# Kernel optimization log

Hardware: AMD Instinct MI355X
Metric: run time of the kernel (lower is better)

## Reference

```python
import jax, jax.numpy as jnp
import numpy as np

T, H, I, E = 4096, 1024, 512, 16


def setup_inputs() -> dict:
    key = jax.random.key(0)
    k1, k2, k3 = jax.random.split(key, 3)
    x = jax.random.normal(k1, (T, H), dtype=jnp.float32)
    gate_up_proj = jax.random.normal(k2, (E, H, 2 * I), dtype=jnp.float32) * 0.02
    down_proj = jax.random.normal(k3, (E, I, H), dtype=jnp.float32) * 0.02
    # uneven expert token counts summing exactly to T (no padding rows)
    rng = np.random.default_rng(0)
    raw = rng.integers(64, 512, size=E)
    counts = (raw * T) // raw.sum()
    counts[-1] += T - counts.sum()
    num_tokens_per_expert = jnp.asarray(counts, dtype=jnp.int32)
    return {"x": x, "gate_up_proj": gate_up_proj, "down_proj": down_proj,
            "num_tokens_per_expert": num_tokens_per_expert}


def reference(x, gate_up_proj, down_proj, num_tokens_per_expert):
    # tokens are sorted by expert; build per-token expert id (jit-safe: fixed length)
    n_tok = x.shape[0]
    n_exp = gate_up_proj.shape[0]
    seg = jnp.repeat(jnp.arange(n_exp), num_tokens_per_expert, total_repeat_length=n_tok)  # [T]

    def body(acc, ew):
        e, w_gu, w_d = ew
        xe = jnp.where((seg == e)[:, None], x, jnp.zeros((), x.dtype))  # [T, H], zero rows for other experts
        gu = xe @ w_gu                                                  # [T, 2I]
        g, u = jnp.split(gu, 2, axis=-1)
        o = (jax.nn.silu(g) * u) @ w_d                                  # [T, H]; masked rows stay exactly 0
        return acc + o, None

    init = jnp.zeros((n_tok, down_proj.shape[-1]), x.dtype)
    out, _ = jax.lax.scan(body, init, (jnp.arange(n_exp), gate_up_proj, down_proj))
    return out
```

## Files before the change

kernel.cpp:

```cpp
#include <hip/hip_runtime.h>
#include <hip/hip_bf16.h>

#define T_TOK 4096
#define H_DIM 1024
#define I_DIM 512
#define E_EXP 16
#define BM    128
#define BK    64
#define BSTR  68

using bf16x8   = __attribute__((ext_vector_type(8))) short;
using floatx4  = __attribute__((ext_vector_type(4))) float;
using ushort4v = __attribute__((ext_vector_type(4))) unsigned short;

__device__ __forceinline__ unsigned short f2bf(float f) {
  union { float f; unsigned u; } v; v.f = f;
  return (unsigned short)((v.u + 0x7FFFu + ((v.u >> 16) & 1u)) >> 16);
}
__device__ __forceinline__ unsigned pk2(float a, float b) {
  return (unsigned)f2bf(a) | ((unsigned)f2bf(b) << 16);
}

__device__ __forceinline__ void gld16(const void* g, void* l) {
  __builtin_amdgcn_global_load_lds((const __attribute__((address_space(1))) void*)g,
                                   (__attribute__((address_space(3))) void*)l,
                                   16, 0, 0);
}

__device__ __forceinline__ bool tile_info(const int* __restrict__ counts, int by,
                                          int& e, int& row0, int& base, int& cnt) {
  int acc = 0, off = 0;
  e = -1;
  #pragma unroll
  for (int i = 0; i < E_EXP; ++i) {
    int c = counts[i];
    int nt = (c + BM - 1) >> 7;
    if (e < 0 && by < acc + nt) { e = i; row0 = (by - acc) * BM; base = off; cnt = c; }
    acc += nt; off += c;
  }
  return e >= 0;
}

__global__ void k_cvt(const float* __restrict__ x, unsigned short* __restrict__ xb) {
  const float4* s4 = (const float4*)x;
  int b0 = blockIdx.x * 512 + threadIdx.x;
  float4 a = s4[b0];
  float4 b = s4[b0 + 256];
  ushort4v oa, ob;
  oa.x = f2bf(a.x); oa.y = f2bf(a.y); oa.z = f2bf(a.z); oa.w = f2bf(a.w);
  ob.x = f2bf(b.x); ob.y = f2bf(b.y); ob.z = f2bf(b.z); ob.w = f2bf(b.w);
  ((ushort4v*)xb)[b0] = oa;
  ((ushort4v*)xb)[b0 + 256] = ob;
}

__launch_bounds__(256, 3)
__global__ void k_gemm_a(const unsigned short* __restrict__ xb,
                         const float* __restrict__ wgu,
                         unsigned short* __restrict__ hb,
                         const int* __restrict__ counts) {
  __shared__ unsigned short As[BM * BK];
  __shared__ unsigned short Bs[BM * BSTR];

  int e, row0, base, cnt;
  if (!tile_info(counts, blockIdx.y, e, row0, base, cnt)) return;
  const int rows = (cnt - row0 < BM) ? (cnt - row0) : BM;
  const int c0 = blockIdx.x * 64;

  const int tid = threadIdx.x;
  const int w = tid >> 6, l = tid & 63;
  const int lr = l & 15, q = l >> 4;
  const int asr = l >> 3, akc = (l & 7) * 8;
  const int nloc = ((w & 1) << 6) | l;
  const int kh = (w >> 1) * 32;
  const int gcol = (nloc < 64) ? (c0 + nloc) : (I_DIM + c0 + (nloc - 64));
  const float* wcol = wgu + (size_t)e * H_DIM * (2 * I_DIM) + gcol;
  unsigned int* BsD = (unsigned int*)Bs;
  const int bdst = nloc * (BSTR / 2) + (kh >> 1);

  const int mhalf = w & 1, nhalf = w >> 1;
  const int mrow = mhalf * 64;

  floatx4 accg[4][2], accu[4][2];
  #pragma unroll
  for (int i = 0; i < 4; ++i)
    #pragma unroll
    for (int j = 0; j < 2; ++j) { accg[i][j] = (floatx4){0,0,0,0}; accu[i][j] = (floatx4){0,0,0,0}; }

  const int nk = H_DIM / BK;
  for (int ki = 0; ki < nk; ++ki) {
    const int kk = ki * BK;
    float bv[32];
    #pragma unroll
    for (int j = 0; j < 32; ++j)
      bv[j] = wcol[(size_t)(kk + kh + j) * (2 * I_DIM)];
    #pragma unroll
    for (int t = 0; t < 4; ++t) {
      int r = w * 32 + t * 8 + asr;
      int gr = r < rows ? r : rows - 1;
      gld16(&xb[(size_t)(base + row0 + gr) * H_DIM + kk + akc], &As[(w * 32 + t * 8) * BK]);
    }
    #pragma unroll
    for (int jq = 0; jq < 8; ++jq) {
      uint2 d;
      d.x = pk2(bv[4 * jq + 0], bv[4 * jq + 1]);
      d.y = pk2(bv[4 * jq + 2], bv[4 * jq + 3]);
      *(uint2*)&BsD[bdst + jq * 2] = d;
    }
    __syncthreads();
    #pragma unroll
    for (int kf = 0; kf < 2; ++kf) {
      const int ch = (kf * 4 + q) * 8;
      bf16x8 af[4], bg[2], bu[2];
      #pragma unroll
      for (int mi = 0; mi < 4; ++mi)
        af[mi] = *(const bf16x8*)&As[(mrow + mi * 16 + lr) * BK + ch];
      #pragma unroll
      for (int ni = 0; ni < 2; ++ni) {
        bg[ni] = *(const bf16x8*)&Bs[(nhalf * 32 + ni * 16 + lr) * BSTR + ch];
        bu[ni] = *(const bf16x8*)&Bs[(64 + nhalf * 32 + ni * 16 + lr) * BSTR + ch];
      }
      #pragma unroll
      for (int mi = 0; mi < 4; ++mi)
        #pragma unroll
        for (int ni = 0; ni < 2; ++ni) {
          accg[mi][ni] = __builtin_amdgcn_mfma_f32_16x16x32_bf16(af[mi], bg[ni], accg[mi][ni], 0, 0, 0);
          accu[mi][ni] = __builtin_amdgcn_mfma_f32_16x16x32_bf16(af[mi], bu[ni], accu[mi][ni], 0, 0, 0);
        }
    }
    __syncthreads();
  }

  #pragma unroll
  for (int mi = 0; mi < 4; ++mi)
    #pragma unroll
    for (int r = 0; r < 4; ++r) {
      int row_local = mrow + mi * 16 + q * 4 + r;
      if (row_local >= rows) continue;
      size_t orow = (size_t)(base + row0 + row_local) * I_DIM;
      #pragma unroll
      for (int ni = 0; ni < 2; ++ni) {
        float g = accg[mi][ni][r], u = accu[mi][ni][r];
        float s = g / (1.0f + __expf(-g)) * u;
        hb[orow + c0 + nhalf * 32 + ni * 16 + lr] = f2bf(s);
      }
    }
}

__launch_bounds__(256, 3)
__global__ void k_gemm_b(const unsigned short* __restrict__ hb,
                         const float* __restrict__ wdn,
                         float* __restrict__ out,
                         const int* __restrict__ counts) {
  __shared__ unsigned short As[BM * BK];
  __shared__ unsigned short Bs[BM * BSTR];

  int e, row0, base, cnt;
  if (!tile_info(counts, blockIdx.y, e, row0, base, cnt)) return;
  const int rows = (cnt - row0 < BM) ? (cnt - row0) : BM;
  const int n0 = blockIdx.x * 128;

  const int tid = threadIdx.x;
  const int w = tid >> 6, l = tid & 63;
  const int lr = l & 15, q = l >> 4;
  const int asr = l >> 3, akc = (l & 7) * 8;
  const int nloc = ((w & 1) << 6) | l;
  const int kh = (w >> 1) * 32;
  const float* wcol = wdn + (size_t)e * I_DIM * H_DIM + n0 + nloc;
  unsigned int* BsD = (unsigned int*)Bs;
  const int bdst = nloc * (BSTR / 2) + (kh >> 1);

  const int mhalf = w & 1, nhalf = w >> 1;
  const int mrow = mhalf * 64;

  floatx4 acc[4][4];
  #pragma unroll
  for (int i = 0; i < 4; ++i)
    #pragma unroll
    for (int j = 0; j < 4; ++j) acc[i][j] = (floatx4){0,0,0,0};

  const int nk = I_DIM / BK;
  for (int ki = 0; ki < nk; ++ki) {
    const int kk = ki * BK;
    float bv[32];
    #pragma unroll
    for (int j = 0; j < 32; ++j)
      bv[j] = wcol[(size_t)(kk + kh + j) * H_DIM];
    #pragma unroll
    for (int t = 0; t < 4; ++t) {
      int r = w * 32 + t * 8 + asr;
      int gr = r < rows ? r : rows - 1;
      gld16(&hb[(size_t)(base + row0 + gr) * I_DIM + kk + akc], &As[(w * 32 + t * 8) * BK]);
    }
    #pragma unroll
    for (int jq = 0; jq < 8; ++jq) {
      uint2 d;
      d.x = pk2(bv[4 * jq + 0], bv[4 * jq + 1]);
      d.y = pk2(bv[4 * jq + 2], bv[4 * jq + 3]);
      *(uint2*)&BsD[bdst + jq * 2] = d;
    }
    __syncthreads();
    #pragma unroll
    for (int kf = 0; kf < 2; ++kf) {
      const int ch = (kf * 4 + q) * 8;
      bf16x8 af[4], bf[4];
      #pragma unroll
      for (int mi = 0; mi < 4; ++mi)
        af[mi] = *(const bf16x8*)&As[(mrow + mi * 16 + lr) * BK + ch];
      #pragma unroll
      for (int ni = 0; ni < 4; ++ni)
        bf[ni] = *(const bf16x8*)&Bs[(nhalf * 64 + ni * 16 + lr) * BSTR + ch];
      #pragma unroll
      for (int mi = 0; mi < 4; ++mi)
        #pragma unroll
        for (int ni = 0; ni < 4; ++ni)
          acc[mi][ni] = __builtin_amdgcn_mfma_f32_16x16x32_bf16(af[mi], bf[ni], acc[mi][ni], 0, 0, 0);
    }
    __syncthreads();
  }

  #pragma unroll
  for (int mi = 0; mi < 4; ++mi)
    #pragma unroll
    for (int r = 0; r < 4; ++r) {
      int row_local = mrow + mi * 16 + q * 4 + r;
      if (row_local >= rows) continue;
      size_t orow = (size_t)(base + row0 + row_local) * H_DIM;
      #pragma unroll
      for (int ni = 0; ni < 4; ++ni)
        out[orow + n0 + nhalf * 64 + ni * 16 + lr] = acc[mi][ni][r];
    }
}

extern "C" void kernel_launch(void* const* d_in, const int* in_sizes, int n_in,
                              void* d_out, int out_size, void* d_ws, size_t ws_size,
                              hipStream_t stream) {
  const float* x      = (const float*)d_in[0];
  const float* wgu    = (const float*)d_in[1];
  const float* wdn    = (const float*)d_in[2];
  const int*   counts = (const int*)d_in[3];
  float* out = (float*)d_out;

  unsigned char* ws = (unsigned char*)d_ws;
  unsigned short* xb = (unsigned short*)(ws);
  unsigned short* hb = (unsigned short*)(ws + 8388608);

  k_cvt<<<2048, 256, 0, stream>>>(x, xb);
  k_gemm_a<<<dim3(I_DIM / 64, 48), 256, 0, stream>>>(xb, wgu, hb, counts);
  k_gemm_b<<<dim3(H_DIM / 128, 48), 256, 0, stream>>>(hb, wdn, out, counts);
}
```

Measured before the change: 182.0 us.

## Double-buffer A tiles and prefetch weights to overlap loads with MFMA

Both grouped GEMM kernels now prefetch the next K-slice (fp32 weights into registers, bf16 activations into a second LDS buffer via global_load_lds) before computing on the current slice. The goal is to hide global memory latency behind MFMA work. The A tile in LDS also gets an XOR swizzle on 16-byte chunks to cut bank conflicts on fragment reads. The cost is more LDS per block, which may lower occupancy below the launch-bounds target, plus two barriers per iteration.

```diff
diff --git a/kernel.cpp b/kernel.cpp
--- a/kernel.cpp
+++ b/kernel.cpp
@@ -1,5 +1,4 @@
 #include <hip/hip_runtime.h>
-#include <hip/hip_bf16.h>
 
 #define T_TOK 4096
 #define H_DIM 1024
@@ -58,7 +57,7 @@
                          const float* __restrict__ wgu,
                          unsigned short* __restrict__ hb,
                          const int* __restrict__ counts) {
-  __shared__ unsigned short As[BM * BK];
+  __shared__ unsigned short As[2][BM * BK];
   __shared__ unsigned short Bs[BM * BSTR];
 
   int e, row0, base, cnt;
@@ -69,7 +68,9 @@
   const int tid = threadIdx.x;
   const int w = tid >> 6, l = tid & 63;
   const int lr = l & 15, q = l >> 4;
-  const int asr = l >> 3, akc = (l & 7) * 8;
+  const int asr = l >> 3;
+  const int akc = ((l & 7) ^ asr) * 8;
+  const int cswz = lr & 7;
   const int nloc = ((w & 1) << 6) | l;
   const int kh = (w >> 1) * 32;
   const int gcol = (nloc < 64) ? (c0 + nloc) : (I_DIM + c0 + (nloc - 64));
@@ -79,6 +80,14 @@
 
   const int mhalf = w & 1, nhalf = w >> 1;
   const int mrow = mhalf * 64;
+  const unsigned short* arow = xb + (size_t)(base + row0) * H_DIM;
+
+  int agr[4];
+  #pragma unroll
+  for (int t = 0; t < 4; ++t) {
+    int r = w * 32 + t * 8 + asr;
+    agr[t] = (r < rows) ? r : rows - 1;
+  }
 
   floatx4 accg[4][2], accu[4][2];
   #pragma unroll
@@ -86,34 +95,32 @@
     #pragma unroll
     for (int j = 0; j < 2; ++j) { accg[i][j] = (floatx4){0,0,0,0}; accu[i][j] = (floatx4){0,0,0,0}; }
 
-  const int nk = H_DIM / BK;
-  for (int ki = 0; ki < nk; ++ki) {
-    const int kk = ki * BK;
-    float bv[32];
-    #pragma unroll
-    for (int j = 0; j < 32; ++j)
-      bv[j] = wcol[(size_t)(kk + kh + j) * (2 * I_DIM)];
-    #pragma unroll
-    for (int t = 0; t < 4; ++t) {
-      int r = w * 32 + t * 8 + asr;
-      int gr = r < rows ? r : rows - 1;
-      gld16(&xb[(size_t)(base + row0 + gr) * H_DIM + kk + akc], &As[(w * 32 + t * 8) * BK]);
-    }
-    #pragma unroll
-    for (int jq = 0; jq < 8; ++jq) {
-      uint2 d;
-      d.x = pk2(bv[4 * jq + 0], bv[4 * jq + 1]);
-      d.y = pk2(bv[4 * jq + 2], bv[4 * jq + 3]);
-      *(uint2*)&BsD[bdst + jq * 2] = d;
-    }
-    __syncthreads();
+  float bv[32];
+
+  #pragma unroll
+  for (int j = 0; j < 32; ++j) bv[j] = wcol[(size_t)(kh + j) * (2 * I_DIM)];
+  #pragma unroll
+  for (int t = 0; t < 4; ++t)
+    gld16(&arow[(size_t)agr[t] * H_DIM + akc], &As[0][(w * 32 + t * 8) * BK]);
+  #pragma unroll
+  for (int jq = 0; jq < 8; ++jq) {
+    uint2 d;
+    d.x = pk2(bv[4 * jq + 0], bv[4 * jq + 1]);
+    d.y = pk2(bv[4 * jq + 2], bv[4 * jq + 3]);
+    *(uint2*)&BsD[bdst + jq * 2] = d;
+  }
+  __syncthreads();
+
+  auto compute = [&](int cb) {
     #pragma unroll
     for (int kf = 0; kf < 2; ++kf) {
-      const int ch = (kf * 4 + q) * 8;
+      const int c = kf * 4 + q;
+      const int ca = (c ^ cswz) * 8;
+      const int ch = c * 8;
       bf16x8 af[4], bg[2], bu[2];
       #pragma unroll
       for (int mi = 0; mi < 4; ++mi)
-        af[mi] = *(const bf16x8*)&As[(mrow + mi * 16 + lr) * BK + ch];
+        af[mi] = *(const bf16x8*)&As[cb][(mrow + mi * 16 + lr) * BK + ca];
       #pragma unroll
       for (int ni = 0; ni < 2; ++ni) {
         bg[ni] = *(const bf16x8*)&Bs[(nhalf * 32 + ni * 16 + lr) * BSTR + ch];
@@ -127,8 +134,30 @@
           accu[mi][ni] = __builtin_amdgcn_mfma_f32_16x16x32_bf16(af[mi], bu[ni], accu[mi][ni], 0, 0, 0);
         }
     }
+  };
+
+  const int nk = H_DIM / BK;
+  int cur = 0;
+  for (int ki = 0; ki < nk - 1; ++ki) {
+    const int kk = (ki + 1) * BK;
+    #pragma unroll
+    for (int j = 0; j < 32; ++j) bv[j] = wcol[(size_t)(kk + kh + j) * (2 * I_DIM)];
+    #pragma unroll
+    for (int t = 0; t < 4; ++t)
+      gld16(&arow[(size_t)agr[t] * H_DIM + kk + akc], &As[cur ^ 1][(w * 32 + t * 8) * BK]);
+    compute(cur);
     __syncthreads();
-  }
+    #pragma unroll
+    for (int jq = 0; jq < 8; ++jq) {
+      uint2 d;
+      d.x = pk2(bv[4 * jq + 0], bv[4 * jq + 1]);
+      d.y = pk2(bv[4 * jq + 2], bv[4 * jq + 3]);
+      *(uint2*)&BsD[bdst + jq * 2] = d;
+    }
+    __syncthreads();
+    cur ^= 1;
+  }
+  compute(cur);
 
   #pragma unroll
   for (int mi = 0; mi < 4; ++mi)
@@ -151,7 +180,7 @@
                          const float* __restrict__ wdn,
                          float* __restrict__ out,
                          const int* __restrict__ counts) {
-  __shared__ unsigned short As[BM * BK];
+  __shared__ unsigned short As[2][BM * BK];
   __shared__ unsigned short Bs[BM * BSTR];
 
   int e, row0, base, cnt;
@@ -162,7 +191,9 @@
   const int tid = threadIdx.x;
   const int w = tid >> 6, l = tid & 63;
   const int lr = l & 15, q = l >> 4;
-  const int asr = l >> 3, akc = (l & 7) * 8;
+  const int asr = l >> 3;
+  const int akc = ((l & 7) ^ asr) * 8;
+  const int cswz = lr & 7;
   const int nloc = ((w & 1) << 6) | l;
   const int kh = (w >> 1) * 32;
   const float* wcol = wdn + (size_t)e * I_DIM * H_DIM + n0 + nloc;
@@ -171,6 +202,14 @@
 
   const int mhalf = w & 1, nhalf = w >> 1;
   const int mrow = mhalf * 64;
+  const unsigned short* arow = hb + (size_t)(base + row0) * I_DIM;
+
+  int agr[4];
+  #pragma unroll
+  for (int t = 0; t < 4; ++t) {
+    int r = w * 32 + t * 8 + asr;
+    agr[t] = (r < rows) ? r : rows - 1;
+  }
 
   floatx4 acc[4][4];
   #pragma unroll
@@ -178,19 +217,54 @@
     #pragma unroll
     for (int j = 0; j < 4; ++j) acc[i][j] = (floatx4){0,0,0,0};
 
+  float bv[32];
+
+  #pragma unroll
+  for (int j = 0; j < 32; ++j) bv[j] = wcol[(size_t)(kh + j) * H_DIM];
+  #pragma unroll
+  for (int t = 0; t < 4; ++t)
+    gld16(&arow[(size_t)agr[t] * I_DIM + akc], &As[0][(w * 32 + t * 8) * BK]);
+  #pragma unroll
+  for (int jq = 0; jq < 8; ++jq) {
+    uint2 d;
+    d.x = pk2(bv[4 * jq + 0], bv[4 * jq + 1]);
+    d.y = pk2(bv[4 * jq + 2], bv[4 * jq + 3]);
+    *(uint2*)&BsD[bdst + jq * 2] = d;
+  }
+  __syncthreads();
+
+  auto compute = [&](int cb) {
+    #pragma unroll
+    for (int kf = 0; kf < 2; ++kf) {
+      const int c = kf * 4 + q;
+      const int ca = (c ^ cswz) * 8;
+      const int ch = c * 8;
+      bf16x8 af[4], bf[4];
+      #pragma unroll
+      for (int mi = 0; mi < 4; ++mi)
+        af[mi] = *(const bf16x8*)&As[cb][(mrow + mi * 16 + lr) * BK + ca];
+      #pragma unroll
+      for (int ni = 0; ni < 4; ++ni)
+        bf[ni] = *(const bf16x8*)&Bs[(nhalf * 64 + ni * 16 + lr) * BSTR + ch];
+      #pragma unroll
+      for (int mi = 0; mi < 4; ++mi)
+        #pragma unroll
+        for (int ni = 0; ni < 4; ++ni)
+          acc[mi][ni] = __builtin_amdgcn_mfma_f32_16x16x32_bf16(af[mi], bf[ni], acc[mi][ni], 0, 0, 0);
+    }
+  };
+
   const int nk = I_DIM / BK;
-  for (int ki = 0; ki < nk; ++ki) {
-    const int kk = ki * BK;
-    float bv[32];
-    #pragma unroll
-    for (int j = 0; j < 32; ++j)
-      bv[j] = wcol[(size_t)(kk + kh + j) * H_DIM];
-    #pragma unroll
-    for (int t = 0; t < 4; ++t) {
-      int r = w * 32 + t * 8 + asr;
-      int gr = r < rows ? r : rows - 1;
-      gld16(&hb[(size_t)(base + row0 + gr) * I_DIM + kk + akc], &As[(w * 32 + t * 8) * BK]);
-    }
+  int cur = 0;
+  for (int ki = 0; ki < nk - 1; ++ki) {
+    const int kk = (ki + 1) * BK;
+    #pragma unroll
+    for (int j = 0; j < 32; ++j) bv[j] = wcol[(size_t)(kk + kh + j) * H_DIM];
+    #pragma unroll
+    for (int t = 0; t < 4; ++t)
+      gld16(&arow[(size_t)agr[t] * I_DIM + kk + akc], &As[cur ^ 1][(w * 32 + t * 8) * BK]);
+    compute(cur);
+    __syncthreads();
     #pragma unroll
     for (int jq = 0; jq < 8; ++jq) {
       uint2 d;
@@ -199,24 +273,9 @@
       *(uint2*)&BsD[bdst + jq * 2] = d;
     }
     __syncthreads();
-    #pragma unroll
-    for (int kf = 0; kf < 2; ++kf) {
-      const int ch = (kf * 4 + q) * 8;
-      bf16x8 af[4], bf[4];
-      #pragma unroll
-      for (int mi = 0; mi < 4; ++mi)
-        af[mi] = *(const bf16x8*)&As[(mrow + mi * 16 + lr) * BK + ch];
-      #pragma unroll
-      for (int ni = 0; ni < 4; ++ni)
-        bf[ni] = *(const bf16x8*)&Bs[(nhalf * 64 + ni * 16 + lr) * BSTR + ch];
-      #pragma unroll
-      for (int mi = 0; mi < 4; ++mi)
-        #pragma unroll
-        for (int ni = 0; ni < 4; ++ni)
-          acc[mi][ni] = __builtin_amdgcn_mfma_f32_16x16x32_bf16(af[mi], bf[ni], acc[mi][ni], 0, 0, 0);
-    }
-    __syncthreads();
-  }
+    cur ^= 1;
+  }
+  compute(cur);
 
   #pragma unroll
   for (int mi = 0; mi < 4; ++mi)
```

Measured after the change: 188.8 us. 3.7% more time.
